# Performance work log

Measured on AMD Instinct MI355X. Metric: run time of the kernel, lower is better.

Reference implementation:

```python
import jax, jax.numpy as jnp
import numpy as np

B, T, D, H = 512, 256, 256, 1024


def setup_inputs() -> dict:
    key = jax.random.key(0)
    ks = jax.random.split(key, 8)
    s = 1.0 / np.sqrt(3 * D)
    return {
        "X": jax.random.normal(ks[0], (B, T, D), dtype=jnp.float32),
        "M": (jax.random.uniform(ks[1], (B, T, D)) < 0.5).astype(jnp.float32),
        "input_means": jax.random.normal(ks[2], (D,), dtype=jnp.float32) * 0.1,
        "gamma_x": jnp.ones((D,), dtype=jnp.float32),
        "Wz": jax.random.normal(ks[3], (H, 3 * D), dtype=jnp.float32) * s,
        "bz": jnp.zeros((H,), dtype=jnp.float32),
        "Wr": jax.random.normal(ks[4], (H, 3 * D), dtype=jnp.float32) * s,
        "br": jnp.zeros((H,), dtype=jnp.float32),
        "Wh": jax.random.normal(ks[5], (H, 3 * D), dtype=jnp.float32) * s,
        "bh": jnp.zeros((H,), dtype=jnp.float32),
        "Wout": jax.random.normal(ks[6], (1, H), dtype=jnp.float32) * (1.0 / np.sqrt(H)),
        "bout": jnp.zeros((1,), dtype=jnp.float32),
    }


def reference(X, M, input_means, gamma_x, Wz, bz, Wr, br, Wh, bh, Wout, bout):
    Bc, Tc, Dc = X.shape
    xm = input_means  # [D], broadcast as the per-timestep mean
    xm_b = jnp.broadcast_to(xm, (Bc, Dc))

    def step(h, xt_mt):
        x_t, m_t = xt_mt  # each [B, D]
        x_hat = m_t * x_t + (1.0 - m_t) * xm
        g = jnp.exp(-gamma_x * (1.0 - m_t))  # input decay
        x_tilde = g * x_hat + (1.0 - g) * xm
        inp = jnp.concatenate([x_tilde, xm_b, m_t], axis=1)  # [B, 3D]
        z_t = jax.nn.sigmoid(inp @ Wz.T + bz)
        r_t = jax.nn.sigmoid(inp @ Wr.T + br)  # computed but unused (faithful to source)
        h_til = jnp.tanh(inp @ Wh.T + bh)
        h_new = (1.0 - z_t) * h + z_t * h_til
        return h_new, None

    h0 = jnp.zeros((Bc, Wz.shape[0]), dtype=X.dtype)
    # scan over time: only the final hidden state feeds the output head
    h_last, _ = jax.lax.scan(step, h0, (jnp.swapaxes(X, 0, 1), jnp.swapaxes(M, 0, 1)))
    out = jax.nn.sigmoid(h_last @ Wout.T + bout)  # [B, 1]
    return out.squeeze(1)  # [B]
```

## Files before the change

kernel.cpp:

```cpp
#include <hip/hip_runtime.h>
#include <cstdint>
#include <cstddef>

#define B_  512
#define T_  256
#define D_  256
#define H_  1024
#define K2  512
#define N2  2048
#define TC  32
#define NCHUNK 8

#define OFF_WB    ((size_t)0)
#define OFF_CVEC  ((size_t)2097152)
#define OFF_H     ((size_t)2105344)
#define OFF_PQ    ((size_t)4202496)
#define OFF_INP2  ((size_t)37756928)

typedef short   bf16x8 __attribute__((ext_vector_type(8)));
typedef float   f32x4  __attribute__((ext_vector_type(4)));

__device__ __forceinline__ unsigned short f2bf(float f) {
    unsigned int u = __float_as_uint(f);
    u += 0x7fffu + ((u >> 16) & 1u);
    return (unsigned short)(u >> 16);
}
__device__ __forceinline__ void async16(const void* g, void* l) {
    __builtin_amdgcn_global_load_lds(
        (const __attribute__((address_space(1))) void*)g,
        (__attribute__((address_space(3))) void*)l, 16, 0, 0);
}

__global__ void build_wb(const float* __restrict__ Wz, const float* __restrict__ Wh,
                         const float* __restrict__ xm, unsigned short* __restrict__ Wb) {
    int id  = blockIdx.x * 256 + threadIdx.x;
    int kq  = id & 3;
    int row = (id >> 2) & 255;
    int ks  = (id >> 10) & 15;
    int nt  = id >> 14;
    int rW  = nt * 256 + row;
    int m   = rW >> 1;
    const float* W = (rW & 1) ? (Wh + (size_t)m * 768) : (Wz + (size_t)m * 768);
    int k = ks * 32 + kq * 8;
    unsigned short o[8];
    #pragma unroll
    for (int j = 0; j < 8; j++) {
        float v;
        if (k < D_) v = W[k + j];
        else { int d = k - D_ + j; v = W[2 * D_ + d] - W[d] * xm[d]; }
        o[j] = f2bf(v);
    }
    uint4 pk;
    pk.x = (unsigned)o[0] | ((unsigned)o[1] << 16);
    pk.y = (unsigned)o[2] | ((unsigned)o[3] << 16);
    pk.z = (unsigned)o[4] | ((unsigned)o[5] << 16);
    pk.w = (unsigned)o[6] | ((unsigned)o[7] << 16);
    size_t dst = ((size_t)(nt * 16 + ks) * 256 + row) * 32
               + (size_t)((kq ^ ((row >> 1) & 3)) * 8);
    *(uint4*)(Wb + dst) = pk;
}

__global__ void build_cvec(const float* __restrict__ Wz, const float* __restrict__ bz,
                           const float* __restrict__ Wh, const float* __restrict__ bh,
                           const float* __restrict__ xm, float* __restrict__ cvec) {
    int r = blockIdx.x;
    int m = r >> 1;
    int d = threadIdx.x;
    const float* W = (r & 1) ? (Wh + (size_t)m * 768) : (Wz + (size_t)m * 768);
    float v = (W[d] + W[D_ + d]) * xm[d];
    for (int off = 32; off; off >>= 1) v += __shfl_down(v, off);
    __shared__ float red[4];
    if ((d & 63) == 0) red[d >> 6] = v;
    __syncthreads();
    if (d == 0) {
        float bias = (r & 1) ? bh[m] : bz[m];
        cvec[r] = bias + red[0] + red[1] + red[2] + red[3];
    }
}

__global__ void build_inp2(const float* __restrict__ X, const float* __restrict__ Mm,
                           unsigned short* __restrict__ inp2) {
    int id  = blockIdx.x * 256 + threadIdx.x;
    int kq  = id & 3;
    int row = (id >> 2) & 127;
    int ks  = (id >> 9) & 15;
    int p   = id >> 13;
    int b   = (p & 127) * 4 + (row >> 5);
    int t   = (p >> 7) * 32 + (row & 31);
    int k   = ks * 32 + kq * 8;
    const size_t rbase = ((size_t)b * T_ + t) * D_;
    unsigned short o[8];
    if (k < D_) {
        const float4* xp = (const float4*)(X  + rbase + k);
        const float4* mp = (const float4*)(Mm + rbase + k);
        float4 x0 = xp[0], x1 = xp[1], m0 = mp[0], m1 = mp[1];
        o[0]=f2bf(m0.x*x0.x); o[1]=f2bf(m0.y*x0.y); o[2]=f2bf(m0.z*x0.z); o[3]=f2bf(m0.w*x0.w);
        o[4]=f2bf(m1.x*x1.x); o[5]=f2bf(m1.y*x1.y); o[6]=f2bf(m1.z*x1.z); o[7]=f2bf(m1.w*x1.w);
    } else {
        const float4* mp = (const float4*)(Mm + rbase + (k - D_));
        float4 m0 = mp[0], m1 = mp[1];
        o[0]=f2bf(m0.x); o[1]=f2bf(m0.y); o[2]=f2bf(m0.z); o[3]=f2bf(m0.w);
        o[4]=f2bf(m1.x); o[5]=f2bf(m1.y); o[6]=f2bf(m1.z); o[7]=f2bf(m1.w);
    }
    uint4 pk;
    pk.x = (unsigned)o[0] | ((unsigned)o[1] << 16);
    pk.y = (unsigned)o[2] | ((unsigned)o[3] << 16);
    pk.z = (unsigned)o[4] | ((unsigned)o[5] << 16);
    pk.w = (unsigned)o[6] | ((unsigned)o[7] << 16);
    size_t dst = ((size_t)(p * 16 + ks) * 128 + row) * 32
               + (size_t)((kq ^ ((row >> 1) & 3)) * 8);
    *(uint4*)(inp2 + dst) = pk;
}

__global__ __launch_bounds__(512, 4) void gemm_scan(
    const unsigned short* __restrict__ A,
    const unsigned short* __restrict__ Wb,
    const float* __restrict__ cvec,
    float2* __restrict__ PQ)
{
    __shared__ __align__(16) unsigned short sm[36864];
    const int tid  = threadIdx.x;
    const int lane = tid & 63;
    const int w    = tid >> 6;
    const int blk  = blockIdx.x;
    const int p    = (blk >> 6) * 8 + (blk & 7);
    const int nt   = (blk >> 3) & 7;
    const int c    = p >> 7;
    const int bg0  = (p & 127) * 4;

    const unsigned short* asrc = A  + (size_t)p  * 65536  + tid * 8;
    const unsigned short* bsrc = Wb + (size_t)nt * 131072 + tid * 8;

    const int wm = w >> 2, wn = w & 3;
    const int l15 = lane & 15, q = lane >> 4;

    int aoff[4], boff[4];
    #pragma unroll
    for (int i = 0; i < 4; i++) {
        int row = wm * 64 + i * 16 + l15;
        aoff[i] = row * 32 + ((q ^ ((row >> 1) & 3)) * 8);
    }
    #pragma unroll
    for (int j = 0; j < 4; j++) {
        int rt = wn * 64 + j * 16 + l15;
        boff[j] = rt * 32 + ((q ^ ((rt >> 1) & 3)) * 8);
    }

#define STAGE(rng, ks_)                                                          \
    { async16(asrc + (ks_) * 4096,        sm + (rng) * 4096 + w * 512);          \
      async16(bsrc + (size_t)(ks_) * 8192,        sm + 12288 + (rng) * 8192 + w * 512); \
      async16(bsrc + (size_t)(ks_) * 8192 + 4096, sm + 12288 + (rng) * 8192 + 4096 + w * 512); }

    f32x4 acc[4][4] = {};

    STAGE(0, 0);
    STAGE(1, 1);

    #pragma unroll
    for (int ks = 0; ks < 16; ++ks) {
        const int cur = ks % 3;
        if (ks + 2 < 16) STAGE((ks + 2) % 3, ks + 2);
        if (ks < 14)       asm volatile("s_waitcnt vmcnt(6)" ::: "memory");
        else if (ks == 14) asm volatile("s_waitcnt vmcnt(3)" ::: "memory");
        else               asm volatile("s_waitcnt vmcnt(0)" ::: "memory");
        asm volatile("s_barrier" ::: "memory");

        bf16x8 af[4], bv[4];
        #pragma unroll
        for (int i = 0; i < 4; i++)
            af[i] = *(const bf16x8*)&sm[cur * 4096 + aoff[i]];
        #pragma unroll
        for (int j = 0; j < 4; j++)
            bv[j] = *(const bf16x8*)&sm[12288 + cur * 8192 + boff[j]];
        __builtin_amdgcn_s_setprio(1);
        #pragma unroll
        for (int i = 0; i < 4; i++)
            #pragma unroll
            for (int j = 0; j < 4; j++)
                acc[i][j] = __builtin_amdgcn_mfma_f32_16x16x32_bf16(af[i], bv[j], acc[i][j], 0, 0, 0);
        __builtin_amdgcn_s_setprio(0);
        asm volatile("s_barrier" ::: "memory");
    }
#undef STAGE

    const float par = (float)(lane & 1);
    const float sg  = 1.f + par;
    #pragma unroll
    for (int j = 0; j < 4; ++j) {
        const int ncol = nt * 256 + wn * 64 + j * 16 + l15;
        const float cadd = cvec[ncol];
        #pragma unroll
        for (int bl2 = 0; bl2 < 2; ++bl2) {
            float PA = 1.f, QA = 0.f, PB = 1.f, QB = 0.f;
            #pragma unroll
            for (int r = 0; r < 4; ++r) {
                {
                    float v  = acc[bl2 * 2][j][r] + cadd;
                    float a  = sg * __builtin_amdgcn_rcpf(1.f + __expf(-sg * v)) - par;
                    float ap = __shfl_xor(a, 1);
                    float z  = (lane & 1) ? ap : a;
                    float ht = (lane & 1) ? a : ap;
                    float om = 1.f - z;
                    QA = om * QA + z * ht;
                    PA = om * PA;
                }
                {
                    float v  = acc[bl2 * 2 + 1][j][r] + cadd;
                    float a  = sg * __builtin_amdgcn_rcpf(1.f + __expf(-sg * v)) - par;
                    float ap = __shfl_xor(a, 1);
                    float z  = (lane & 1) ? ap : a;
                    float ht = (lane & 1) ? a : ap;
                    float om = 1.f - z;
                    QB = om * QB + z * ht;
                    PB = om * PB;
                }
            }
            #pragma unroll
            for (int s = 16; s <= 32; s <<= 1) {
                float PAp = __shfl_xor(PA, s), QAp = __shfl_xor(QA, s);
                float PBp = __shfl_xor(PB, s), QBp = __shfl_xor(QB, s);
                const bool late = (lane & s) != 0;
                float Pe = late ? PAp : PA,  Qe = late ? QAp : QA;
                float Pl = late ? PA  : PAp, Ql = late ? QA  : QAp;
                PA = Pl * Pe;  QA = Pl * Qe + Ql;
                Pe = late ? PBp : PB;  Qe = late ? QBp : QB;
                Pl = late ? PB  : PBp; Ql = late ? QB  : QBp;
                PB = Pl * Pe;  QB = Pl * Qe + Ql;
            }
            const float Ptot = PB * PA;
            const float Qtot = PB * QA + QB;
            if ((q == bl2 * 2) && ((lane & 1) == 0)) {
                const int npg = ncol >> 1;
                const int bgl = bg0 + wm * 2 + bl2;
                PQ[((size_t)c * B_ + bgl) * H_ + npg] = make_float2(Ptot, Qtot);
            }
        }
    }
}

__global__ void combine(const float2* __restrict__ PQ, float* __restrict__ hbuf) {
    int v = blockIdx.x * 256 + threadIdx.x;
    int b = v >> 10;
    int n = v & 1023;
    float h = 0.f;
    #pragma unroll
    for (int c = 0; c < NCHUNK; c++) {
        float2 pq = PQ[((size_t)c * B_ + b) * H_ + n];
        h = pq.x * h + pq.y;
    }
    hbuf[(size_t)b * H_ + n] = h;
}

__global__ void head(const float* __restrict__ hbuf, const float* __restrict__ Wout,
                     const float* __restrict__ bout, float* __restrict__ out) {
    int b = blockIdx.x;
    float s = 0.f;
    for (int n = threadIdx.x; n < H_; n += 256)
        s += hbuf[(size_t)b * H_ + n] * Wout[n];
    for (int off = 32; off; off >>= 1) s += __shfl_down(s, off);
    __shared__ float red[4];
    if ((threadIdx.x & 63) == 0) red[threadIdx.x >> 6] = s;
    __syncthreads();
    if (threadIdx.x == 0) {
        float t = red[0] + red[1] + red[2] + red[3] + bout[0];
        out[b] = 1.f / (1.f + expf(-t));
    }
}

extern "C" void kernel_launch(void* const* d_in, const int* in_sizes, int n_in,
                              void* d_out, int out_size, void* d_ws, size_t ws_size,
                              hipStream_t stream) {
    const float* X    = (const float*)d_in[0];
    const float* Mm   = (const float*)d_in[1];
    const float* xm   = (const float*)d_in[2];
    const float* Wz   = (const float*)d_in[4];
    const float* bz   = (const float*)d_in[5];
    const float* Wh   = (const float*)d_in[8];
    const float* bh   = (const float*)d_in[9];
    const float* Wout = (const float*)d_in[10];
    const float* bout = (const float*)d_in[11];
    float* out = (float*)d_out;

    char* ws = (char*)d_ws;
    unsigned short* Wb    = (unsigned short*)(ws + OFF_WB);
    float*          cvec  = (float*)(ws + OFF_CVEC);
    float*          hbuf  = (float*)(ws + OFF_H);
    float2*         PQ    = (float2*)(ws + OFF_PQ);
    unsigned short* inp2  = (unsigned short*)(ws + OFF_INP2);

    build_wb  <<<dim3(512),  dim3(256), 0, stream>>>(Wz, Wh, xm, Wb);
    build_cvec<<<dim3(N2),   dim3(256), 0, stream>>>(Wz, bz, Wh, bh, xm, cvec);
    build_inp2<<<dim3(32768), dim3(256), 0, stream>>>(X, Mm, inp2);

    gemm_scan<<<dim3(8192), dim3(512), 0, stream>>>(inp2, Wb, cvec, PQ);

    combine<<<dim3(B_ * H_ / 256), dim3(256), 0, stream>>>(PQ, hbuf);
    head   <<<dim3(B_),            dim3(256), 0, stream>>>(hbuf, Wout, bout, out);
}
```

Baseline: 696.1 us.

## Load GEMM A operand straight to registers and quad-buffer B in LDS

The input matrix is now written row-major instead of in a swizzled tile layout. The GEMM loads its A fragments directly from global memory into double-buffered registers, bypassing shared memory. Only the weight tiles are staged in LDS, now in four buffers, which lets the trailing per-iteration barrier be dropped. The aim is to cut LDS traffic and barrier cost. In exchange it adds redundant, less-coalesced global reads of A across the waves that share it, and higher register pressure.

Result: slower. 860.9 us (+23.7%).

```diff
diff --git a/kernel.cpp b/kernel.cpp
--- a/kernel.cpp
+++ b/kernel.cpp
@@ -81,13 +81,12 @@
 __global__ void build_inp2(const float* __restrict__ X, const float* __restrict__ Mm,
                            unsigned short* __restrict__ inp2) {
     int id  = blockIdx.x * 256 + threadIdx.x;
-    int kq  = id & 3;
-    int row = (id >> 2) & 127;
-    int ks  = (id >> 9) & 15;
+    int k8  = id & 63;
+    int row = (id >> 6) & 127;
     int p   = id >> 13;
     int b   = (p & 127) * 4 + (row >> 5);
     int t   = (p >> 7) * 32 + (row & 31);
-    int k   = ks * 32 + kq * 8;
+    int k   = k8 * 8;
     const size_t rbase = ((size_t)b * T_ + t) * D_;
     unsigned short o[8];
     if (k < D_) {
@@ -107,9 +106,7 @@
     pk.y = (unsigned)o[2] | ((unsigned)o[3] << 16);
     pk.z = (unsigned)o[4] | ((unsigned)o[5] << 16);
     pk.w = (unsigned)o[6] | ((unsigned)o[7] << 16);
-    size_t dst = ((size_t)(p * 16 + ks) * 128 + row) * 32
-               + (size_t)((kq ^ ((row >> 1) & 3)) * 8);
-    *(uint4*)(inp2 + dst) = pk;
+    *(uint4*)(inp2 + ((size_t)p * 128 + row) * 512 + k) = pk;
 }
 
 __global__ __launch_bounds__(512, 4) void gemm_scan(
@@ -118,7 +115,7 @@
     const float* __restrict__ cvec,
     float2* __restrict__ PQ)
 {
-    __shared__ __align__(16) unsigned short sm[36864];
+    __shared__ __align__(16) unsigned short sm[32768];
     const int tid  = threadIdx.x;
     const int lane = tid & 63;
     const int w    = tid >> 6;
@@ -128,60 +125,58 @@
     const int c    = p >> 7;
     const int bg0  = (p & 127) * 4;
 
-    const unsigned short* asrc = A  + (size_t)p  * 65536  + tid * 8;
-    const unsigned short* bsrc = Wb + (size_t)nt * 131072 + tid * 8;
-
     const int wm = w >> 2, wn = w & 3;
     const int l15 = lane & 15, q = lane >> 4;
 
-    int aoff[4], boff[4];
-    #pragma unroll
-    for (int i = 0; i < 4; i++) {
-        int row = wm * 64 + i * 16 + l15;
-        aoff[i] = row * 32 + ((q ^ ((row >> 1) & 3)) * 8);
-    }
+    const unsigned short* bsrc  = Wb + (size_t)nt * 131072 + tid * 8;
+    const unsigned short* abase = A + (size_t)p * 65536
+                                + (size_t)(wm * 64 + l15) * 512 + q * 8;
+
+    int boff[4];
     #pragma unroll
     for (int j = 0; j < 4; j++) {
         int rt = wn * 64 + j * 16 + l15;
         boff[j] = rt * 32 + ((q ^ ((rt >> 1) & 3)) * 8);
     }
 
-#define STAGE(rng, ks_)                                                          \
-    { async16(asrc + (ks_) * 4096,        sm + (rng) * 4096 + w * 512);          \
-      async16(bsrc + (size_t)(ks_) * 8192,        sm + 12288 + (rng) * 8192 + w * 512); \
-      async16(bsrc + (size_t)(ks_) * 8192 + 4096, sm + 12288 + (rng) * 8192 + 4096 + w * 512); }
+#define STAGEB(rng, ks_)                                                        \
+    { async16(bsrc + (ks_) * 8192,        sm + (rng) * 8192 + tid * 8);         \
+      async16(bsrc + (ks_) * 8192 + 4096, sm + (rng) * 8192 + 4096 + tid * 8); }
+#define LOADA(buf, ks_)                                                         \
+    { _Pragma("unroll")                                                         \
+      for (int i = 0; i < 4; i++)                                               \
+          af[buf][i] = *(const bf16x8*)(abase + i * 8192 + (ks_) * 32); }
 
     f32x4 acc[4][4] = {};
-
-    STAGE(0, 0);
-    STAGE(1, 1);
+    bf16x8 af[2][4];
+
+    STAGEB(0, 0);
+    STAGEB(1, 1);
+    LOADA(0, 0);
 
     #pragma unroll
     for (int ks = 0; ks < 16; ++ks) {
-        const int cur = ks % 3;
-        if (ks + 2 < 16) STAGE((ks + 2) % 3, ks + 2);
+        if (ks + 2 < 16) STAGEB((ks + 2) & 3, ks + 2);
+        if (ks + 1 < 16) LOADA((ks + 1) & 1, ks + 1);
         if (ks < 14)       asm volatile("s_waitcnt vmcnt(6)" ::: "memory");
-        else if (ks == 14) asm volatile("s_waitcnt vmcnt(3)" ::: "memory");
+        else if (ks == 14) asm volatile("s_waitcnt vmcnt(4)" ::: "memory");
         else               asm volatile("s_waitcnt vmcnt(0)" ::: "memory");
         asm volatile("s_barrier" ::: "memory");
 
-        bf16x8 af[4], bv[4];
-        #pragma unroll
-        for (int i = 0; i < 4; i++)
-            af[i] = *(const bf16x8*)&sm[cur * 4096 + aoff[i]];
+        bf16x8 bv[4];
         #pragma unroll
         for (int j = 0; j < 4; j++)
-            bv[j] = *(const bf16x8*)&sm[12288 + cur * 8192 + boff[j]];
+            bv[j] = *(const bf16x8*)&sm[(ks & 3) * 8192 + boff[j]];
         __builtin_amdgcn_s_setprio(1);
         #pragma unroll
         for (int i = 0; i < 4; i++)
             #pragma unroll
             for (int j = 0; j < 4; j++)
-                acc[i][j] = __builtin_amdgcn_mfma_f32_16x16x32_bf16(af[i], bv[j], acc[i][j], 0, 0, 0);
+                acc[i][j] = __builtin_amdgcn_mfma_f32_16x16x32_bf16(af[ks & 1][i], bv[j], acc[i][j], 0, 0, 0);
         __builtin_amdgcn_s_setprio(0);
-        asm volatile("s_barrier" ::: "memory");
-    }
-#undef STAGE
+    }
+#undef STAGEB
+#undef LOADA
 
     const float par = (float)(lane & 1);
     const float sg  = 1.f + par;
```
